# Kernel optimization log

Measured on AMD Instinct MI355X. Metric: run time of the kernel, lower is better.

Reference implementation:

```python
import jax, jax.numpy as jnp
import numpy as np

EPS_BN = 1e-5


def _batchnorm(h, g, b):
    # training-mode BatchNorm1d over the flattened (B*N*k) axis
    mu = jnp.mean(h, axis=0)
    var = jnp.var(h, axis=0)
    return g * (h - mu) * jax.lax.rsqrt(var + EPS_BN) + b


def setup_inputs() -> dict:
    key = jax.random.key(0)
    ks = jax.random.split(key, 5)
    B, N = 4, 8192
    x = jax.random.normal(ks[0], (B, N, 3), dtype=jnp.float32)
    W1 = jax.random.normal(ks[1], (7, 10), dtype=jnp.float32) * (1.0 / np.sqrt(7.0))
    b1 = jax.random.normal(ks[2], (10,), dtype=jnp.float32) * 0.01
    W2 = jax.random.normal(ks[3], (10, 10), dtype=jnp.float32) * (1.0 / np.sqrt(10.0))
    b2 = jax.random.normal(ks[4], (10,), dtype=jnp.float32) * 0.01
    g1 = jnp.ones((10,), jnp.float32); be1 = jnp.zeros((10,), jnp.float32)
    g2 = jnp.ones((10,), jnp.float32); be2 = jnp.zeros((10,), jnp.float32)
    return {"x": x, "W1": W1, "b1": b1, "g1": g1, "be1": be1,
            "W2": W2, "b2": b2, "g2": g2, "be2": be2, "k": 9}


def reference(x, W1, b1, g1, be1, W2, b2, g2, be2, k):
    B, N, C = x.shape
    # --- kNN graph (brute force, self included as nearest) ---
    sq = jnp.sum(x * x, axis=-1)                                    # (B,N)
    d2 = sq[:, :, None] + sq[:, None, :] - 2.0 * jnp.einsum('bnc,bmc->bnm', x, x)
    _, idx = jax.lax.top_k(-d2, k + 1)                              # (B,N,k+1)
    nbrs = x[jnp.arange(B)[:, None, None], idx]                     # (B,N,k+1,3)
    rel = (nbrs - x[:, :, None, :])[:, :, 1:, :]                    # drop self -> (B,N,k,3)
    # --- sort neighbors by azimuth phi = atan2(y, x) ---
    phi = jnp.arctan2(rel[..., 1], rel[..., 0])                     # (B,N,k)
    order = jnp.argsort(phi, axis=-1)
    v1 = jnp.take_along_axis(rel, order[..., None], axis=2)         # (B,N,k,3)
    v2 = jnp.roll(v1, -1, axis=2)                                   # next neighbor (cyclic)
    # --- umbrella-style surface features ---
    centroids = 0.5 * (v1 + v2)
    normals = jnp.cross(v1, v2)
    normals = normals / (jnp.linalg.norm(normals, axis=-1, keepdims=True) + 1e-6)
    sign = jnp.where(normals[..., 0:1, 0] > 0, 1.0, -1.0)[..., None]  # (B,N,1,1)
    normals = normals * sign
    position = jnp.sum(normals * centroids, axis=-1, keepdims=True) / jnp.sqrt(jnp.asarray(3.0, x.dtype))
    feat = jnp.concatenate([centroids, normals, position], axis=-1)   # (B,N,k,7)
    feat = feat.reshape(B * N * k, 7)
    # --- tiny MLP + max-pool over k ---
    h = jax.nn.relu(_batchnorm(feat @ W1 + b1, g1, be1))
    h = jax.nn.relu(_batchnorm(h @ W2 + b2, g2, be2))
    return jnp.max(h.reshape(B, N, k, 10), axis=2)                  # (B,N,10)
```

## Files before the change

kernel.cpp:

```cpp
#include <hip/hip_runtime.h>
#include <math.h>
#include <float.h>
#include <stdint.h>

#define B_ 4
#define N_ 8192
#define K_ 9
#define NPTS (B_ * N_)
#define NROWS (NPTS * K_)
#define SPLIT 8
#define CHUNK (N_ / SPLIT)
#define NGROUP 32
#define GSIZE (CHUNK / NGROUP)
#define GSTRIDE 33
#define NCOPY 16

typedef float f4 __attribute__((ext_vector_type(4)));
typedef float f32x2 __attribute__((ext_vector_type(2)));

__device__ __forceinline__ f32x2 dist2_pk(f32x2 xx, f32x2 yy, f32x2 zz, f32x2 ww,
                                          f32x2 qx, f32x2 qy, f32x2 qz, f32x2 qw) {
  f32x2 t0 = qx * xx;
  f32x2 t1 = __builtin_elementwise_fma(qy, yy, t0);
  f32x2 t2 = __builtin_elementwise_fma(qz, zz, t1);
  f32x2 s  = qw + ww;
  f32x2 m2 = {-2.0f, -2.0f};
  return __builtin_elementwise_fma(t2, m2, s);
}

#define GDECL(G) float gd##G; int gi##G;
#define SCANG(G)                                                           \
  { float bgd = FLT_MAX; int bq = 0;                                       \
    _Pragma("clang loop unroll(disable)")                                  \
    for (int pr = 0; pr < 16; pr += 4) {                                   \
      const f4* cp = CH + (G * GSTRIDE + 2 * pr);                          \
      f4 A0 = cp[0], B0 = cp[1], A1 = cp[2], B1 = cp[3];                   \
      f4 A2 = cp[4], B2 = cp[5], A3 = cp[6], B3 = cp[7];                   \
      f32x2 dA = dist2_pk(__builtin_shufflevector(A0, A0, 0, 1),           \
                          __builtin_shufflevector(A0, A0, 2, 3),           \
                          __builtin_shufflevector(B0, B0, 0, 1),           \
                          __builtin_shufflevector(B0, B0, 2, 3),           \
                          qx2, qy2, qz2, qw2);                             \
      f32x2 dB = dist2_pk(__builtin_shufflevector(A1, A1, 0, 1),           \
                          __builtin_shufflevector(A1, A1, 2, 3),           \
                          __builtin_shufflevector(B1, B1, 0, 1),           \
                          __builtin_shufflevector(B1, B1, 2, 3),           \
                          qx2, qy2, qz2, qw2);                             \
      f32x2 dC = dist2_pk(__builtin_shufflevector(A2, A2, 0, 1),           \
                          __builtin_shufflevector(A2, A2, 2, 3),           \
                          __builtin_shufflevector(B2, B2, 0, 1),           \
                          __builtin_shufflevector(B2, B2, 2, 3),           \
                          qx2, qy2, qz2, qw2);                             \
      f32x2 dD = dist2_pk(__builtin_shufflevector(A3, A3, 0, 1),           \
                          __builtin_shufflevector(A3, A3, 2, 3),           \
                          __builtin_shufflevector(B3, B3, 0, 1),           \
                          __builtin_shufflevector(B3, B3, 2, 3),           \
                          qx2, qy2, qz2, qw2);                             \
      float d0 = dA.x, d1 = dA.y, d2 = dB.x, d3 = dB.y;                    \
      float d4 = dC.x, d5 = dC.y, d6 = dD.x, d7 = dD.y;                    \
      if (HS) {                                                            \
        int j = G * GSIZE + 2 * pr;                                        \
        d0 = (j + 0 == nl) ? FLT_MAX : d0;                                 \
        d1 = (j + 1 == nl) ? FLT_MAX : d1;                                 \
        d2 = (j + 2 == nl) ? FLT_MAX : d2;                                 \
        d3 = (j + 3 == nl) ? FLT_MAX : d3;                                 \
        d4 = (j + 4 == nl) ? FLT_MAX : d4;                                 \
        d5 = (j + 5 == nl) ? FLT_MAX : d5;                                 \
        d6 = (j + 6 == nl) ? FLT_MAX : d6;                                 \
        d7 = (j + 7 == nl) ? FLT_MAX : d7;                                 \
      }                                                                    \
      float m = fminf(fminf(fminf(d0, d1), fminf(d2, d3)),                 \
                      fminf(fminf(d4, d5), fminf(d6, d7)));                \
      bool lt = m < bgd; bgd = lt ? m : bgd; bq = lt ? pr : bq;            \
    }                                                                      \
    gd##G = bgd; gi##G = -1 - bq; }
#define LMC(G, S)                                                          \
  { bool lt = gd##G < wd##S;                                               \
    wd##S = lt ? gd##G : wd##S; wi##S = lt ? gi##G : wi##S;                \
    wg##S = lt ? G : wg##S; }
#define CMB(S)                                                             \
  { bool lt = wd##S < wda;                                                 \
    wda = lt ? wd##S : wda; wia = lt ? wi##S : wia; wga = lt ? wg##S : wga; }
#define WBK(G)                                                             \
  { bool m = (wg == G); gd##G = m ? nd : gd##G; gi##G = m ? ni : gi##G; }

#define TOURN8()                                                           \
  float e01d, e23d, e45d, e67d, f03d, f47d, md;                            \
  int   e01i, e23i, e45i, e67i, f03i, f47i, mi;                            \
  { bool t;                                                                \
    t = d1 < d0; e01d = t ? d1 : d0; e01i = t ? (j + 1) : (j + 0);         \
    t = d3 < d2; e23d = t ? d3 : d2; e23i = t ? (j + 3) : (j + 2);         \
    t = d5 < d4; e45d = t ? d5 : d4; e45i = t ? (j + 5) : (j + 4);         \
    t = d7 < d6; e67d = t ? d7 : d6; e67i = t ? (j + 7) : (j + 6);         \
    t = e23d < e01d; f03d = t ? e23d : e01d; f03i = t ? e23i : e01i;       \
    t = e67d < e45d; f47d = t ? e67d : e45d; f47i = t ? e67i : e45i;       \
    t = f47d < f03d; md = t ? f47d : f03d; mi = t ? f47i : f03i; }

template <bool HS>
__device__ __forceinline__ void knn_chunk(const f4* CH, f32x2 qx2, f32x2 qy2,
                                          f32x2 qz2, f32x2 qw2,
                                          int nl, int j0, int s, int p,
                                          uint2* __restrict__ PBDI) {
  GDECL(0) GDECL(1) GDECL(2) GDECL(3) GDECL(4) GDECL(5) GDECL(6) GDECL(7)
  GDECL(8) GDECL(9) GDECL(10) GDECL(11) GDECL(12) GDECL(13) GDECL(14) GDECL(15)
  GDECL(16) GDECL(17) GDECL(18) GDECL(19) GDECL(20) GDECL(21) GDECL(22) GDECL(23)
  GDECL(24) GDECL(25) GDECL(26) GDECL(27) GDECL(28) GDECL(29) GDECL(30) GDECL(31)

  SCANG(0) SCANG(1) SCANG(2) SCANG(3) SCANG(4) SCANG(5) SCANG(6) SCANG(7)
  SCANG(8) SCANG(9) SCANG(10) SCANG(11) SCANG(12) SCANG(13) SCANG(14) SCANG(15)
  SCANG(16) SCANG(17) SCANG(18) SCANG(19) SCANG(20) SCANG(21) SCANG(22) SCANG(23)
  SCANG(24) SCANG(25) SCANG(26) SCANG(27) SCANG(28) SCANG(29) SCANG(30) SCANG(31)

#pragma clang loop unroll(disable)
  for (int r = 0; r < K_; ++r) {
    float wda = gd0; int wia = gi0; int wga = 0;
    LMC(1,a) LMC(2,a) LMC(3,a) LMC(4,a) LMC(5,a) LMC(6,a) LMC(7,a)
    float wdb = gd8; int wib = gi8; int wgb = 8;
    LMC(9,b) LMC(10,b) LMC(11,b) LMC(12,b) LMC(13,b) LMC(14,b) LMC(15,b)
    float wdc = gd16; int wic = gi16; int wgc = 16;
    LMC(17,c) LMC(18,c) LMC(19,c) LMC(20,c) LMC(21,c) LMC(22,c) LMC(23,c)
    float wdd = gd24; int wid = gi24; int wgd = 24;
    LMC(25,d) LMC(26,d) LMC(27,d) LMC(28,d) LMC(29,d) LMC(30,d) LMC(31,d)
    CMB(b) CMB(c) CMB(d)
    float wd = wda; int wist = wia; int wg = wga;

    int ab = wg * GSTRIDE;
    int jb = wg * GSIZE;

    int wi;
    {
      int bq = (wist >= 0) ? 0 : (-1 - wist);
      const f4* cp = CH + (ab + 2 * bq);
      f4 A0 = cp[0], B0 = cp[1], A1 = cp[2], B1 = cp[3];
      f4 A2 = cp[4], B2 = cp[5], A3 = cp[6], B3 = cp[7];
      int j = jb + 2 * bq;
      f32x2 dA = dist2_pk(__builtin_shufflevector(A0, A0, 0, 1),
                          __builtin_shufflevector(A0, A0, 2, 3),
                          __builtin_shufflevector(B0, B0, 0, 1),
                          __builtin_shufflevector(B0, B0, 2, 3),
                          qx2, qy2, qz2, qw2);
      f32x2 dB = dist2_pk(__builtin_shufflevector(A1, A1, 0, 1),
                          __builtin_shufflevector(A1, A1, 2, 3),
                          __builtin_shufflevector(B1, B1, 0, 1),
                          __builtin_shufflevector(B1, B1, 2, 3),
                          qx2, qy2, qz2, qw2);
      f32x2 dC = dist2_pk(__builtin_shufflevector(A2, A2, 0, 1),
                          __builtin_shufflevector(A2, A2, 2, 3),
                          __builtin_shufflevector(B2, B2, 0, 1),
                          __builtin_shufflevector(B2, B2, 2, 3),
                          qx2, qy2, qz2, qw2);
      f32x2 dD = dist2_pk(__builtin_shufflevector(A3, A3, 0, 1),
                          __builtin_shufflevector(A3, A3, 2, 3),
                          __builtin_shufflevector(B3, B3, 0, 1),
                          __builtin_shufflevector(B3, B3, 2, 3),
                          qx2, qy2, qz2, qw2);
      float d0 = dA.x, d1 = dA.y, d2 = dB.x, d3 = dB.y;
      float d4 = dC.x, d5 = dC.y, d6 = dD.x, d7 = dD.y;
      if (HS) {
        d0 = (j + 0 == nl) ? FLT_MAX : d0;
        d1 = (j + 1 == nl) ? FLT_MAX : d1;
        d2 = (j + 2 == nl) ? FLT_MAX : d2;
        d3 = (j + 3 == nl) ? FLT_MAX : d3;
        d4 = (j + 4 == nl) ? FLT_MAX : d4;
        d5 = (j + 5 == nl) ? FLT_MAX : d5;
        d6 = (j + 6 == nl) ? FLT_MAX : d6;
        d7 = (j + 7 == nl) ? FLT_MAX : d7;
      }
      const int IMX = 0x7fffffff;
      int a0 = (d0 == wd) ? (j + 0) : IMX;
      int a1 = (d1 == wd) ? (j + 1) : IMX;
      int a2 = (d2 == wd) ? (j + 2) : IMX;
      int a3 = (d3 == wd) ? (j + 3) : IMX;
      int a4 = (d4 == wd) ? (j + 4) : IMX;
      int a5 = (d5 == wd) ? (j + 5) : IMX;
      int a6 = (d6 == wd) ? (j + 6) : IMX;
      int a7 = (d7 == wd) ? (j + 7) : IMX;
      int m01 = a0 < a1 ? a0 : a1;
      int m23 = a2 < a3 ? a2 : a3;
      int m45 = a4 < a5 ? a4 : a5;
      int m67 = a6 < a7 ? a6 : a7;
      int mA = m01 < m23 ? m01 : m23;
      int mB = m45 < m67 ? m45 : m67;
      int jm = mA < mB ? mA : mB;
      wi = (wist >= 0) ? wist : jm;
    }

    uint2 o; o.x = __float_as_uint(wd); o.y = (unsigned)(j0 + wi);
    PBDI[(size_t)(s * K_ + r) * NPTS + p] = o;

    float nd = FLT_MAX; int ni = 0;
#pragma clang loop unroll(disable)
    for (int pr = 0; pr < 16; pr += 4) {
      const f4* cp = CH + (ab + 2 * pr);
      f4 A0 = cp[0], B0 = cp[1], A1 = cp[2], B1 = cp[3];
      f4 A2 = cp[4], B2 = cp[5], A3 = cp[6], B3 = cp[7];
      int j = jb + 2 * pr;
      f32x2 dA = dist2_pk(__builtin_shufflevector(A0, A0, 0, 1),
                          __builtin_shufflevector(A0, A0, 2, 3),
                          __builtin_shufflevector(B0, B0, 0, 1),
                          __builtin_shufflevector(B0, B0, 2, 3),
                          qx2, qy2, qz2, qw2);
      f32x2 dB = dist2_pk(__builtin_shufflevector(A1, A1, 0, 1),
                          __builtin_shufflevector(A1, A1, 2, 3),
                          __builtin_shufflevector(B1, B1, 0, 1),
                          __builtin_shufflevector(B1, B1, 2, 3),
                          qx2, qy2, qz2, qw2);
      f32x2 dC = dist2_pk(__builtin_shufflevector(A2, A2, 0, 1),
                          __builtin_shufflevector(A2, A2, 2, 3),
                          __builtin_shufflevector(B2, B2, 0, 1),
                          __builtin_shufflevector(B2, B2, 2, 3),
                          qx2, qy2, qz2, qw2);
      f32x2 dD = dist2_pk(__builtin_shufflevector(A3, A3, 0, 1),
                          __builtin_shufflevector(A3, A3, 2, 3),
                          __builtin_shufflevector(B3, B3, 0, 1),
                          __builtin_shufflevector(B3, B3, 2, 3),
                          qx2, qy2, qz2, qw2);
      float d0 = dA.x, d1 = dA.y, d2 = dB.x, d3 = dB.y;
      float d4 = dC.x, d5 = dC.y, d6 = dD.x, d7 = dD.y;
      if (HS) {
        d0 = (j + 0 == nl) ? FLT_MAX : d0;
        d1 = (j + 1 == nl) ? FLT_MAX : d1;
        d2 = (j + 2 == nl) ? FLT_MAX : d2;
        d3 = (j + 3 == nl) ? FLT_MAX : d3;
        d4 = (j + 4 == nl) ? FLT_MAX : d4;
        d5 = (j + 5 == nl) ? FLT_MAX : d5;
        d6 = (j + 6 == nl) ? FLT_MAX : d6;
        d7 = (j + 7 == nl) ? FLT_MAX : d7;
      }
      bool k0 = (d0 > wd) | ((d0 == wd) & ((j + 0) > wi));
      bool k1 = (d1 > wd) | ((d1 == wd) & ((j + 1) > wi));
      bool k2 = (d2 > wd) | ((d2 == wd) & ((j + 2) > wi));
      bool k3 = (d3 > wd) | ((d3 == wd) & ((j + 3) > wi));
      bool k4 = (d4 > wd) | ((d4 == wd) & ((j + 4) > wi));
      bool k5 = (d5 > wd) | ((d5 == wd) & ((j + 5) > wi));
      bool k6 = (d6 > wd) | ((d6 == wd) & ((j + 6) > wi));
      bool k7 = (d7 > wd) | ((d7 == wd) & ((j + 7) > wi));
      d0 = k0 ? d0 : FLT_MAX;
      d1 = k1 ? d1 : FLT_MAX;
      d2 = k2 ? d2 : FLT_MAX;
      d3 = k3 ? d3 : FLT_MAX;
      d4 = k4 ? d4 : FLT_MAX;
      d5 = k5 ? d5 : FLT_MAX;
      d6 = k6 ? d6 : FLT_MAX;
      d7 = k7 ? d7 : FLT_MAX;
      TOURN8();
      bool lt = md < nd; nd = lt ? md : nd; ni = lt ? mi : ni;
    }
    WBK(0) WBK(1) WBK(2) WBK(3) WBK(4) WBK(5) WBK(6) WBK(7)
    WBK(8) WBK(9) WBK(10) WBK(11) WBK(12) WBK(13) WBK(14) WBK(15)
    WBK(16) WBK(17) WBK(18) WBK(19) WBK(20) WBK(21) WBK(22) WBK(23)
    WBK(24) WBK(25) WBK(26) WBK(27) WBK(28) WBK(29) WBK(30) WBK(31)
  }
}

__launch_bounds__(128, 4)
__global__ void k_knn(const float* __restrict__ x, uint2* __restrict__ PBDI,
                      double* __restrict__ ACC) {
  __shared__ f4 CH[NGROUP * GSTRIDE];
  int bid = blockIdx.x;
  if (bid == 0) {
    for (int t = threadIdx.x; t < NCOPY * 40; t += 128) ACC[t] = 0.0;
  }
  int pg = bid >> 3;
  int s = bid & (SPLIT - 1);
  int p = pg * 128 + threadIdx.x;
  int b = p >> 13;
  int n = p & (N_ - 1);
  int bO = b * N_;
  int j0 = s * CHUNK;

  const float* xq = x + 3 * (size_t)p;
  float qa = xq[0], qb = xq[1], qc = xq[2];
  float qw = qa * qa + qb * qb + qc * qc;
  f32x2 qx2 = {qa, qa}, qy2 = {qb, qb}, qz2 = {qc, qc}, qw2 = {qw, qw};

  for (int u = threadIdx.x; u < CHUNK / 2; u += 128) {
    const float* xp = x + 3 * (size_t)(bO + j0 + 2 * u);
    float a0 = xp[0], b0 = xp[1], c0 = xp[2];
    float a1 = xp[3], b1 = xp[4], c1 = xp[5];
    int G = u >> 4, rr = u & 15;
    f4 lo = {a0, a1, b0, b1};
    f4 hi = {c0, c1, a0 * a0 + b0 * b0 + c0 * c0, a1 * a1 + b1 * b1 + c1 * c1};
    CH[G * GSTRIDE + 2 * rr] = lo;
    CH[G * GSTRIDE + 2 * rr + 1] = hi;
  }
  __syncthreads();

  int n0 = (pg * 128) & (N_ - 1);
  int nl = n - j0;
  if (s == (n0 >> 10)) knn_chunk<true >(CH, qx2, qy2, qz2, qw2, nl, j0, s, p, PBDI);
  else                 knn_chunk<false>(CH, qx2, qy2, qz2, qw2, nl, j0, s, p, PBDI);
}

#define LVL(bdv, biv)                                                     \
  { bool lt = cd < (bdv); float td = (bdv); int ti = (biv);               \
    (bdv) = lt ? cd : (bdv); (biv) = lt ? ci : (biv);                     \
    cd = lt ? td : cd; ci = lt ? ti : ci; }
#define INS9ALL()                                                         \
  LVL(b0d, b0i) LVL(b1d, b1i) LVL(b2d, b2i) LVL(b3d, b3i) LVL(b4d, b4i)  \
  LVL(b5d, b5i) LVL(b6d, b6i) LVL(b7d, b7i) LVL(b8d, b8i)
#define TOP9_DECL()                                                       \
  float b0d = FLT_MAX, b1d = FLT_MAX, b2d = FLT_MAX, b3d = FLT_MAX,       \
        b4d = FLT_MAX, b5d = FLT_MAX, b6d = FLT_MAX, b7d = FLT_MAX,       \
        b8d = FLT_MAX;                                                    \
  int b0i = 0, b1i = 0, b2i = 0, b3i = 0, b4i = 0, b5i = 0, b6i = 0,      \
      b7i = 0, b8i = 0;

#define MKREL(T)                                                          \
  float rx##T, ry##T, rz##T, ph##T;                                       \
  { const float* mp = x + 3 * (size_t)(bO + b##T##i);                     \
    rx##T = mp[0] - qa; ry##T = mp[1] - qb; rz##T = mp[2] - qc;           \
    ph##T = atan2f(ry##T, rx##T); }

#define CE(A, Bv)                                                         \
  { bool lt = ph##Bv < ph##A; float t0;                                   \
    t0 = ph##A; ph##A = lt ? ph##Bv : t0; ph##Bv = lt ? t0 : ph##Bv;      \
    t0 = rx##A; rx##A = lt ? rx##Bv : t0; rx##Bv = lt ? t0 : rx##Bv;      \
    t0 = ry##A; ry##A = lt ? ry##Bv : t0; ry##Bv = lt ? t0 : ry##Bv;      \
    t0 = rz##A; rz##A = lt ? rz##Bv : t0; rz##Bv = lt ? t0 : rz##Bv; }

#define ST9(arr, v0, v1, v2, v3, v4, v5, v6, v7, v8)                      \
  arr[0 * 64 + pl] = v0; arr[1 * 64 + pl] = v1; arr[2 * 64 + pl] = v2;    \
  arr[3 * 64 + pl] = v3; arr[4 * 64 + pl] = v4; arr[5 * 64 + pl] = v5;    \
  arr[6 * 64 + pl] = v6; arr[7 * 64 + pl] = v7; arr[8 * 64 + pl] = v8;

__launch_bounds__(256, 4)
__global__ void k_tail1(const float* __restrict__ x, const uint2* __restrict__ PBDI,
                        const float* __restrict__ W1, const float* __restrict__ b1,
                        float* __restrict__ H1, double* __restrict__ ACC) {
  __shared__ float  LMD[64 * 37];
  __shared__ int    LMI[64 * 37];
  __shared__ float  LREL[3][9 * 64];
  __shared__ float  LSGN[64];
  __shared__ double sred[4][20];

  int q = threadIdx.x >> 6;
  int pl = threadIdx.x & 63;
  int pbase = blockIdx.x * 64;
  int p = pbase + pl;

  {
    TOP9_DECL();
#pragma unroll
    for (int e = 0; e < 2 * K_; ++e) {
      uint2 v = PBDI[(size_t)(q * 2 * K_ + e) * NPTS + p];
      float cd = __uint_as_float(v.x);
      int ci = (int)v.y;
      INS9ALL();
    }
    int base = pl * 37 + q * 9;
    LMD[base + 0] = b0d; LMD[base + 1] = b1d; LMD[base + 2] = b2d;
    LMD[base + 3] = b3d; LMD[base + 4] = b4d; LMD[base + 5] = b5d;
    LMD[base + 6] = b6d; LMD[base + 7] = b7d; LMD[base + 8] = b8d;
    LMI[base + 0] = b0i; LMI[base + 1] = b1i; LMI[base + 2] = b2i;
    LMI[base + 3] = b3i; LMI[base + 4] = b4i; LMI[base + 5] = b5i;
    LMI[base + 6] = b6i; LMI[base + 7] = b7i; LMI[base + 8] = b8i;
  }
  __syncthreads();

  if (q == 0) {
    int b = p >> 13;
    int bO = b * N_;
    const float* xq = x + 3 * (size_t)p;
    float qa = xq[0], qb = xq[1], qc = xq[2];

    TOP9_DECL();
#pragma clang loop unroll_count(3)
    for (int e = 0; e < 4 * K_; ++e) {
      float cd = LMD[pl * 37 + e];
      int ci = LMI[pl * 37 + e];
      INS9ALL();
    }

    MKREL(0) MKREL(1) MKREL(2) MKREL(3) MKREL(4)
    MKREL(5) MKREL(6) MKREL(7) MKREL(8)

    CE(0,1)
    CE(1,2) CE(0,1)
    CE(2,3) CE(1,2) CE(0,1)
    CE(3,4) CE(2,3) CE(1,2) CE(0,1)
    CE(4,5) CE(3,4) CE(2,3) CE(1,2) CE(0,1)
    CE(5,6) CE(4,5) CE(3,4) CE(2,3) CE(1,2) CE(0,1)
    CE(6,7) CE(5,6) CE(4,5) CE(3,4) CE(2,3) CE(1,2) CE(0,1)
    CE(7,8) CE(6,7) CE(5,6) CE(4,5) CE(3,4) CE(2,3) CE(1,2) CE(0,1)

    float nx0 = ry0 * rz1 - rz0 * ry1;
    float ny0 = rz0 * rx1 - rx0 * rz1;
    float nz0 = rx0 * ry1 - ry0 * rx1;
    float nrm0 = sqrtf(nx0 * nx0 + ny0 * ny0 + nz0 * nz0) + 1e-6f;
    LSGN[pl] = ((nx0 / nrm0) > 0.0f) ? 1.0f : -1.0f;

    ST9(LREL[0], rx0, rx1, rx2, rx3, rx4, rx5, rx6, rx7, rx8)
    ST9(LREL[1], ry0, ry1, ry2, ry3, ry4, ry5, ry6, ry7, ry8)
    ST9(LREL[2], rz0, rz1, rz2, rz3, rz4, rz5, rz6, rz7, rz8)
  }
  __syncthreads();

  double sum[10], ss[10];
#pragma unroll
  for (int c = 0; c < 10; ++c) { sum[c] = 0.0; ss[c] = 0.0; }

#pragma clang loop unroll(disable)
  for (int rl = threadIdx.x; rl < 9 * 64; rl += 256) {
    int t = rl >> 6;
    int pp = rl & 63;
    int t2 = (t + 1 == K_) ? 0 : t + 1;
    float v1x = LREL[0][t * 64 + pp];
    float v1y = LREL[1][t * 64 + pp];
    float v1z = LREL[2][t * 64 + pp];
    float v2x = LREL[0][t2 * 64 + pp];
    float v2y = LREL[1][t2 * 64 + pp];
    float v2z = LREL[2][t2 * 64 + pp];
    float sgn = LSGN[pp];

    float cx = 0.5f * (v1x + v2x);
    float cy = 0.5f * (v1y + v2y);
    float cz = 0.5f * (v1z + v2z);
    float nx = v1y * v2z - v1z * v2y;
    float ny = v1z * v2x - v1x * v2z;
    float nz = v1x * v2y - v1y * v2x;
    float nrm = sqrtf(nx * nx + ny * ny + nz * nz) + 1e-6f;
    nx /= nrm; ny /= nrm; nz /= nrm;
    nx *= sgn; ny *= sgn; nz *= sgn;
    float pos = (nx * cx + ny * cy + nz * cz) / 1.7320508075688772f;

    float fv[7] = {cx, cy, cz, nx, ny, nz, pos};
#pragma unroll
    for (int c = 0; c < 10; ++c) {
      float h = b1[c];
#pragma unroll
      for (int rr = 0; rr < 7; ++rr) h = fmaf(fv[rr], W1[rr * 10 + c], h);
      H1[(size_t)c * NROWS + (size_t)t * NPTS + pbase + pp] = h;
      double hd = (double)h;
      sum[c] += hd; ss[c] += hd * hd;
    }
  }

  int lane = threadIdx.x & 63, wv = threadIdx.x >> 6;
#pragma unroll
  for (int c = 0; c < 10; ++c) {
    double a = sum[c];
#pragma unroll
    for (int off = 32; off > 0; off >>= 1) a += __shfl_down(a, off);
    if (lane == 0) sred[wv][c] = a;
    double qq = ss[c];
#pragma unroll
    for (int off = 32; off > 0; off >>= 1) qq += __shfl_down(qq, off);
    if (lane == 0) sred[wv][10 + c] = qq;
  }
  __syncthreads();
  if (threadIdx.x < 20) {
    atomicAdd(&ACC[(blockIdx.x & (NCOPY - 1)) * 40 + threadIdx.x],
              sred[0][threadIdx.x] + sred[1][threadIdx.x] +
              sred[2][threadIdx.x] + sred[3][threadIdx.x]);
  }
}

__launch_bounds__(64)
__global__ void k_mlp2(const float* __restrict__ H1, double* __restrict__ ACC,
                       const float* __restrict__ g1, const float* __restrict__ be1,
                       const float* __restrict__ W2, const float* __restrict__ b2,
                       const float* __restrict__ g2, float* __restrict__ EXT) {
  __shared__ float MR[20];
  __shared__ double sred[20];
  if (threadIdx.x < 20) {
    int c = threadIdx.x % 10;
    int half = threadIdx.x / 10;
    double s0 = 0.0, s1 = 0.0;
#pragma unroll
    for (int cc = 0; cc < NCOPY; ++cc) {
      s0 += ACC[cc * 40 + c];
      s1 += ACC[cc * 40 + 10 + c];
    }
    double mu = s0 / (double)NROWS;
    double var = s1 / (double)NROWS - mu * mu;
    MR[threadIdx.x] = half ? (float)(1.0 / sqrt(var + 1e-5)) : (float)mu;
  }
  __syncthreads();

  int p = blockIdx.x * 64 + threadIdx.x;
  double sum[10], ss[10];
  float ext[10], sg[10];
#pragma unroll
  for (int c = 0; c < 10; ++c) {
    sum[c] = 0.0; ss[c] = 0.0;
    sg[c] = g2[c];
    ext[c] = (sg[c] >= 0.0f) ? -FLT_MAX : FLT_MAX;
  }

#pragma unroll
  for (int t = 0; t < K_; ++t) {
    float v[10];
#pragma unroll
    for (int c = 0; c < 10; ++c) {
      float h = H1[(size_t)c * NROWS + (size_t)t * NPTS + p];
      float z = g1[c] * (h - MR[c]) * MR[10 + c] + be1[c];
      v[c] = z > 0.0f ? z : 0.0f;
    }
#pragma unroll
    for (int c = 0; c < 10; ++c) {
      float h = b2[c];
#pragma unroll
      for (int u = 0; u < 10; ++u) h = fmaf(v[u], W2[u * 10 + c], h);
      sum[c] += (double)h;
      ss[c] += (double)h * (double)h;
      ext[c] = (sg[c] >= 0.0f) ? fmaxf(ext[c], h) : fminf(ext[c], h);
    }
  }

#pragma unroll
  for (int c = 0; c < 10; ++c)
    EXT[(size_t)c * NPTS + p] = ext[c];

#pragma unroll
  for (int c = 0; c < 10; ++c) {
    double a = sum[c];
#pragma unroll
    for (int off = 32; off > 0; off >>= 1) a += __shfl_down(a, off);
    if (threadIdx.x == 0) sred[c] = a;
    double qq = ss[c];
#pragma unroll
    for (int off = 32; off > 0; off >>= 1) qq += __shfl_down(qq, off);
    if (threadIdx.x == 0) sred[10 + c] = qq;
  }
  __syncthreads();
  if (threadIdx.x < 20) {
    atomicAdd(&ACC[(blockIdx.x & (NCOPY - 1)) * 40 + 20 + threadIdx.x],
              sred[threadIdx.x]);
  }
}

__launch_bounds__(64)
__global__ void k_out(const float* __restrict__ EXT, const double* __restrict__ ACC,
                      const float* __restrict__ g2, const float* __restrict__ be2,
                      float* __restrict__ out) {
  __shared__ float MR[20];
  if (threadIdx.x < 20) {
    int c = threadIdx.x % 10;
    int half = threadIdx.x / 10;
    double s0 = 0.0, s1 = 0.0;
#pragma unroll
    for (int cc = 0; cc < NCOPY; ++cc) {
      s0 += ACC[cc * 40 + 20 + c];
      s1 += ACC[cc * 40 + 30 + c];
    }
    double mu = s0 / (double)NROWS;
    double var = s1 / (double)NROWS - mu * mu;
    MR[threadIdx.x] = half ? (float)(1.0 / sqrt(var + 1e-5)) : (float)mu;
  }
  __syncthreads();

  int p = blockIdx.x * 64 + threadIdx.x;
#pragma unroll
  for (int c = 0; c < 10; ++c) {
    float h = EXT[(size_t)c * NPTS + p];
    float z = g2[c] * (h - MR[c]) * MR[10 + c] + be2[c];
    z = z > 0.0f ? z : 0.0f;
    out[(size_t)p * 10 + c] = z;
  }
}

extern "C" void kernel_launch(void* const* d_in, const int* in_sizes, int n_in,
                              void* d_out, int out_size, void* d_ws, size_t ws_size,
                              hipStream_t stream) {
  (void)in_sizes; (void)n_in; (void)out_size; (void)ws_size;
  const float* x  = (const float*)d_in[0];
  const float* W1 = (const float*)d_in[1];
  const float* b1 = (const float*)d_in[2];
  const float* g1 = (const float*)d_in[3];
  const float* be1= (const float*)d_in[4];
  const float* W2 = (const float*)d_in[5];
  const float* b2 = (const float*)d_in[6];
  const float* g2 = (const float*)d_in[7];
  const float* be2= (const float*)d_in[8];
  float* out = (float*)d_out;

  char* base = (char*)d_ws;
  uint2*  PBDI = (uint2*)base;
  float*  H1 = (float*)(base + (size_t)SPLIT * K_ * NPTS * 8);
  double* ACC = (double*)(H1 + (size_t)10 * NROWS);
  float*  EXT = (float*)PBDI;

  k_knn<<<(NPTS / 128) * SPLIT, 128, 0, stream>>>(x, PBDI, ACC);
  k_tail1<<<NPTS / 64, 256, 0, stream>>>(x, PBDI, W1, b1, H1, ACC);
  k_mlp2<<<NPTS / 64, 64, 0, stream>>>(H1, ACC, g1, be1, W2, b2, g2, EXT);
  k_out<<<NPTS / 64, 64, 0, stream>>>(EXT, ACC, g2, be2, out);
}
```

Before: 259.1 us.

## Fuse tail kernels into one cooperative kernel with grid syncs

Merges k_tail1, k_mlp2 and k_out into a single cooperative kernel. The first-layer activations stay in shared memory (aliased over the kNN merge buffers) and the per-point max stays in registers, so the global round trips through H1 and EXT and two kernel launches go away. The batchnorm statistics dependencies are handled with grid.sync between phases. This needs all 512 blocks to be co-resident, which is why launch bounds drop to 2 blocks per CU. The grid-wide barriers and the single active wave in the MLP2 phase may cost latency.

```diff
diff --git a/kernel.cpp b/kernel.cpp
--- a/kernel.cpp
+++ b/kernel.cpp
@@ -1,7 +1,10 @@
 #include <hip/hip_runtime.h>
+#include <hip/hip_cooperative_groups.h>
 #include <math.h>
 #include <float.h>
 #include <stdint.h>
+
+namespace cg = cooperative_groups;
 
 #define B_ 4
 #define N_ 8192
@@ -83,7 +86,6 @@
     wda = lt ? wd##S : wda; wia = lt ? wi##S : wia; wga = lt ? wg##S : wga; }
 #define WBK(G)                                                             \
   { bool m = (wg == G); gd##G = m ? nd : gd##G; gi##G = m ? ni : gi##G; }
-
 #define TOURN8()                                                           \
   float e01d, e23d, e45d, e67d, f03d, f47d, md;                            \
   int   e01i, e23i, e45i, e67i, f03i, f47i, mi;                            \
@@ -324,15 +326,25 @@
   arr[3 * 64 + pl] = v3; arr[4 * 64 + pl] = v4; arr[5 * 64 + pl] = v5;    \
   arr[6 * 64 + pl] = v6; arr[7 * 64 + pl] = v7; arr[8 * 64 + pl] = v8;
 
-__launch_bounds__(256, 4)
-__global__ void k_tail1(const float* __restrict__ x, const uint2* __restrict__ PBDI,
+#define ACCLD(i) __hip_atomic_load(&ACC[i], __ATOMIC_RELAXED, __HIP_MEMORY_SCOPE_AGENT)
+
+__launch_bounds__(256, 2)
+__global__ void k_fused(const float* __restrict__ x, const uint2* __restrict__ PBDI,
                         const float* __restrict__ W1, const float* __restrict__ b1,
-                        float* __restrict__ H1, double* __restrict__ ACC) {
-  __shared__ float  LMD[64 * 37];
-  __shared__ int    LMI[64 * 37];
+                        const float* __restrict__ g1, const float* __restrict__ be1,
+                        const float* __restrict__ W2, const float* __restrict__ b2,
+                        const float* __restrict__ g2, const float* __restrict__ be2,
+                        double* __restrict__ ACC, float* __restrict__ out) {
+  cg::grid_group grid = cg::this_grid();
+
+  __shared__ __align__(16) char SMU[23040];
+  float* LMD = (float*)SMU;
+  int*   LMI = (int*)(SMU + 9472);
+  float* H1L = (float*)SMU;
   __shared__ float  LREL[3][9 * 64];
   __shared__ float  LSGN[64];
-  __shared__ double sred[4][20];
+  __shared__ double sredA[4][20];
+  __shared__ float  MR[20];
 
   int q = threadIdx.x >> 6;
   int pl = threadIdx.x & 63;
@@ -341,7 +353,7 @@
 
   {
     TOP9_DECL();
-#pragma unroll
+#pragma clang loop unroll_count(2)
     for (int e = 0; e < 2 * K_; ++e) {
       uint2 v = PBDI[(size_t)(q * 2 * K_ + e) * NPTS + p];
       float cd = __uint_as_float(v.x);
@@ -396,81 +408,78 @@
   }
   __syncthreads();
 
-  double sum[10], ss[10];
-#pragma unroll
-  for (int c = 0; c < 10; ++c) { sum[c] = 0.0; ss[c] = 0.0; }
+  {
+    double sum[10], ss[10];
+#pragma unroll
+    for (int c = 0; c < 10; ++c) { sum[c] = 0.0; ss[c] = 0.0; }
 
 #pragma clang loop unroll(disable)
-  for (int rl = threadIdx.x; rl < 9 * 64; rl += 256) {
-    int t = rl >> 6;
-    int pp = rl & 63;
-    int t2 = (t + 1 == K_) ? 0 : t + 1;
-    float v1x = LREL[0][t * 64 + pp];
-    float v1y = LREL[1][t * 64 + pp];
-    float v1z = LREL[2][t * 64 + pp];
-    float v2x = LREL[0][t2 * 64 + pp];
-    float v2y = LREL[1][t2 * 64 + pp];
-    float v2z = LREL[2][t2 * 64 + pp];
-    float sgn = LSGN[pp];
-
-    float cx = 0.5f * (v1x + v2x);
-    float cy = 0.5f * (v1y + v2y);
-    float cz = 0.5f * (v1z + v2z);
-    float nx = v1y * v2z - v1z * v2y;
-    float ny = v1z * v2x - v1x * v2z;
-    float nz = v1x * v2y - v1y * v2x;
-    float nrm = sqrtf(nx * nx + ny * ny + nz * nz) + 1e-6f;
-    nx /= nrm; ny /= nrm; nz /= nrm;
-    nx *= sgn; ny *= sgn; nz *= sgn;
-    float pos = (nx * cx + ny * cy + nz * cz) / 1.7320508075688772f;
-
-    float fv[7] = {cx, cy, cz, nx, ny, nz, pos};
+    for (int rl = threadIdx.x; rl < 9 * 64; rl += 256) {
+      int t = rl >> 6;
+      int pp = rl & 63;
+      int t2 = (t + 1 == K_) ? 0 : t + 1;
+      float v1x = LREL[0][t * 64 + pp];
+      float v1y = LREL[1][t * 64 + pp];
+      float v1z = LREL[2][t * 64 + pp];
+      float v2x = LREL[0][t2 * 64 + pp];
+      float v2y = LREL[1][t2 * 64 + pp];
+      float v2z = LREL[2][t2 * 64 + pp];
+      float sgn = LSGN[pp];
+
+      float cx = 0.5f * (v1x + v2x);
+      float cy = 0.5f * (v1y + v2y);
+      float cz = 0.5f * (v1z + v2z);
+      float nx = v1y * v2z - v1z * v2y;
+      float ny = v1z * v2x - v1x * v2z;
+      float nz = v1x * v2y - v1y * v2x;
+      float nrm = sqrtf(nx * nx + ny * ny + nz * nz) + 1e-6f;
+      nx /= nrm; ny /= nrm; nz /= nrm;
+      nx *= sgn; ny *= sgn; nz *= sgn;
+      float pos = (nx * cx + ny * cy + nz * cz) / 1.7320508075688772f;
+
+      float fv[7] = {cx, cy, cz, nx, ny, nz, pos};
+#pragma unroll
+      for (int c = 0; c < 10; ++c) {
+        float h = b1[c];
+#pragma unroll
+        for (int rr = 0; rr < 7; ++rr) h = fmaf(fv[rr], W1[rr * 10 + c], h);
+        H1L[c * 576 + t * 64 + pp] = h;
+        double hd = (double)h;
+        sum[c] += hd; ss[c] += hd * hd;
+      }
+    }
+
+    int lane = threadIdx.x & 63, wv = threadIdx.x >> 6;
 #pragma unroll
     for (int c = 0; c < 10; ++c) {
-      float h = b1[c];
-#pragma unroll
-      for (int rr = 0; rr < 7; ++rr) h = fmaf(fv[rr], W1[rr * 10 + c], h);
-      H1[(size_t)c * NROWS + (size_t)t * NPTS + pbase + pp] = h;
-      double hd = (double)h;
-      sum[c] += hd; ss[c] += hd * hd;
-    }
-  }
-
-  int lane = threadIdx.x & 63, wv = threadIdx.x >> 6;
-#pragma unroll
-  for (int c = 0; c < 10; ++c) {
-    double a = sum[c];
-#pragma unroll
-    for (int off = 32; off > 0; off >>= 1) a += __shfl_down(a, off);
-    if (lane == 0) sred[wv][c] = a;
-    double qq = ss[c];
-#pragma unroll
-    for (int off = 32; off > 0; off >>= 1) qq += __shfl_down(qq, off);
-    if (lane == 0) sred[wv][10 + c] = qq;
+      double a = sum[c];
+#pragma unroll
+      for (int off = 32; off > 0; off >>= 1) a += __shfl_down(a, off);
+      if (lane == 0) sredA[wv][c] = a;
+      double qq = ss[c];
+#pragma unroll
+      for (int off = 32; off > 0; off >>= 1) qq += __shfl_down(qq, off);
+      if (lane == 0) sredA[wv][10 + c] = qq;
+    }
   }
   __syncthreads();
   if (threadIdx.x < 20) {
     atomicAdd(&ACC[(blockIdx.x & (NCOPY - 1)) * 40 + threadIdx.x],
-              sred[0][threadIdx.x] + sred[1][threadIdx.x] +
-              sred[2][threadIdx.x] + sred[3][threadIdx.x]);
-  }
-}
-
-__launch_bounds__(64)
-__global__ void k_mlp2(const float* __restrict__ H1, double* __restrict__ ACC,
-                       const float* __restrict__ g1, const float* __restrict__ be1,
-                       const float* __restrict__ W2, const float* __restrict__ b2,
-                       const float* __restrict__ g2, float* __restrict__ EXT) {
-  __shared__ float MR[20];
-  __shared__ double sred[20];
+              sredA[0][threadIdx.x] + sredA[1][threadIdx.x] +
+              sredA[2][threadIdx.x] + sredA[3][threadIdx.x]);
+  }
+
+  __threadfence();
+  grid.sync();
+
   if (threadIdx.x < 20) {
     int c = threadIdx.x % 10;
     int half = threadIdx.x / 10;
     double s0 = 0.0, s1 = 0.0;
 #pragma unroll
     for (int cc = 0; cc < NCOPY; ++cc) {
-      s0 += ACC[cc * 40 + c];
-      s1 += ACC[cc * 40 + 10 + c];
+      s0 += ACCLD(cc * 40 + c);
+      s1 += ACCLD(cc * 40 + 10 + c);
     }
     double mu = s0 / (double)NROWS;
     double var = s1 / (double)NROWS - mu * mu;
@@ -478,71 +487,65 @@
   }
   __syncthreads();
 
-  int p = blockIdx.x * 64 + threadIdx.x;
-  double sum[10], ss[10];
   float ext[10], sg[10];
-#pragma unroll
-  for (int c = 0; c < 10; ++c) {
-    sum[c] = 0.0; ss[c] = 0.0;
-    sg[c] = g2[c];
-    ext[c] = (sg[c] >= 0.0f) ? -FLT_MAX : FLT_MAX;
-  }
-
-#pragma unroll
-  for (int t = 0; t < K_; ++t) {
-    float v[10];
+  if (q == 0) {
+    double sum[10], ss[10];
 #pragma unroll
     for (int c = 0; c < 10; ++c) {
-      float h = H1[(size_t)c * NROWS + (size_t)t * NPTS + p];
-      float z = g1[c] * (h - MR[c]) * MR[10 + c] + be1[c];
-      v[c] = z > 0.0f ? z : 0.0f;
-    }
+      sum[c] = 0.0; ss[c] = 0.0;
+      sg[c] = g2[c];
+      ext[c] = (sg[c] >= 0.0f) ? -FLT_MAX : FLT_MAX;
+    }
+
+#pragma clang loop unroll(disable)
+    for (int t = 0; t < K_; ++t) {
+      float v[10];
+#pragma unroll
+      for (int c = 0; c < 10; ++c) {
+        float h = H1L[c * 576 + t * 64 + pl];
+        float z = g1[c] * (h - MR[c]) * MR[10 + c] + be1[c];
+        v[c] = z > 0.0f ? z : 0.0f;
+      }
+#pragma unroll
+      for (int c = 0; c < 10; ++c) {
+        float h = b2[c];
+#pragma unroll
+        for (int u = 0; u < 10; ++u) h = fmaf(v[u], W2[u * 10 + c], h);
+        sum[c] += (double)h;
+        ss[c] += (double)h * (double)h;
+        ext[c] = (sg[c] >= 0.0f) ? fmaxf(ext[c], h) : fminf(ext[c], h);
+      }
+    }
+
 #pragma unroll
     for (int c = 0; c < 10; ++c) {
-      float h = b2[c];
-#pragma unroll
-      for (int u = 0; u < 10; ++u) h = fmaf(v[u], W2[u * 10 + c], h);
-      sum[c] += (double)h;
-      ss[c] += (double)h * (double)h;
-      ext[c] = (sg[c] >= 0.0f) ? fmaxf(ext[c], h) : fminf(ext[c], h);
-    }
-  }
-
-#pragma unroll
-  for (int c = 0; c < 10; ++c)
-    EXT[(size_t)c * NPTS + p] = ext[c];
-
-#pragma unroll
-  for (int c = 0; c < 10; ++c) {
-    double a = sum[c];
-#pragma unroll
-    for (int off = 32; off > 0; off >>= 1) a += __shfl_down(a, off);
-    if (threadIdx.x == 0) sred[c] = a;
-    double qq = ss[c];
-#pragma unroll
-    for (int off = 32; off > 0; off >>= 1) qq += __shfl_down(qq, off);
-    if (threadIdx.x == 0) sred[10 + c] = qq;
+      double a = sum[c];
+#pragma unroll
+      for (int off = 32; off > 0; off >>= 1) a += __shfl_down(a, off);
+      if (pl == 0) sredA[0][c] = a;
+      double qq = ss[c];
+#pragma unroll
+      for (int off = 32; off > 0; off >>= 1) qq += __shfl_down(qq, off);
+      if (pl == 0) sredA[0][10 + c] = qq;
+    }
   }
   __syncthreads();
   if (threadIdx.x < 20) {
     atomicAdd(&ACC[(blockIdx.x & (NCOPY - 1)) * 40 + 20 + threadIdx.x],
-              sred[threadIdx.x]);
-  }
-}
-
-__launch_bounds__(64)
-__global__ void k_out(const float* __restrict__ EXT, const double* __restrict__ ACC,
-                      const float* __restrict__ g2, const float* __restrict__ be2,
-                      float* __restrict__ out) {
-  __shared__ float MR[20];
+              sredA[0][threadIdx.x]);
+  }
+
+  __threadfence();
+  grid.sync();
+
   if (threadIdx.x < 20) {
     int c = threadIdx.x % 10;
     int half = threadIdx.x / 10;
     double s0 = 0.0, s1 = 0.0;
 #pragma unroll
     for (int cc = 0; cc < NCOPY; ++cc) {
-      s0 += ACC[cc * 40 + 20 + c];
-      s1 += ACC[cc * 40 + 30 + c];
+      s0 += ACCLD(cc * 40 + 20 + c);
+      s1 += ACCLD(cc * 40 + 30 + c);
     }
     double mu = s0 / (double)NROWS;
     double var = s1 / (double)NROWS - mu * mu;
@@ -550,13 +553,13 @@
   }
   __syncthreads();
 
-  int p = blockIdx.x * 64 + threadIdx.x;
-#pragma unroll
-  for (int c = 0; c < 10; ++c) {
-    float h = EXT[(size_t)c * NPTS + p];
-    float z = g2[c] * (h - MR[c]) * MR[10 + c] + be2[c];
-    z = z > 0.0f ? z : 0.0f;
-    out[(size_t)p * 10 + c] = z;
+  if (q == 0) {
+#pragma unroll
+    for (int c = 0; c < 10; ++c) {
+      float z = g2[c] * (ext[c] - MR[c]) * MR[10 + c] + be2[c];
+      z = z > 0.0f ? z : 0.0f;
+      out[(size_t)p * 10 + c] = z;
+    }
   }
 }
 
@@ -577,12 +580,13 @@
 
   char* base = (char*)d_ws;
   uint2*  PBDI = (uint2*)base;
-  float*  H1 = (float*)(base + (size_t)SPLIT * K_ * NPTS * 8);
-  double* ACC = (double*)(H1 + (size_t)10 * NROWS);
-  float*  EXT = (float*)PBDI;
+  double* ACC = (double*)(base + (size_t)SPLIT * K_ * NPTS * 8);
 
   k_knn<<<(NPTS / 128) * SPLIT, 128, 0, stream>>>(x, PBDI, ACC);
-  k_tail1<<<NPTS / 64, 256, 0, stream>>>(x, PBDI, W1, b1, H1, ACC);
-  k_mlp2<<<NPTS / 64, 64, 0, stream>>>(H1, ACC, g1, be1, W2, b2, g2, EXT);
-  k_out<<<NPTS / 64, 64, 0, stream>>>(EXT, ACC, g2, be2, out);
+
+  void* kargs[] = {(void*)&x, (void*)&PBDI, (void*)&W1, (void*)&b1,
+                   (void*)&g1, (void*)&be1, (void*)&W2, (void*)&b2,
+                   (void*)&g2, (void*)&be2, (void*)&ACC, (void*)&out};
+  hipLaunchCooperativeKernel((const void*)k_fused, dim3(NPTS / 64), dim3(256),
+                             kargs, 0, stream);
 }
```

Result: slower. 404.3 us (+56.0%).
